# Performance work log

Hardware: AMD Instinct MI355X
Metric: run time of the kernel (lower is better)

Reference implementation:

```python
import jax, jax.numpy as jnp
import numpy as np

TIME_SEG_LEN = 5
PRED_STEPS = 1
B, N, D = 4, 4096, 4
F1, F2 = 32, 64  # cnn filters; F2 must equal GCSConv/Dense width 64


def _conv1d_time(x, Wc1, bc1, Wc2, bc2):
    # x: [B, N, T, D] -> per-node temporal CNN collapsing T=5 -> 1 -> [B, N, F2]
    b, n, t, d = x.shape
    xr = x.reshape(b * n, t, d)
    dn = ('NWC', 'WIO', 'NWC')
    h = jax.lax.conv_general_dilated(xr, Wc1, (1,), 'VALID', dimension_numbers=dn) + bc1
    h = jax.nn.relu(h)
    h = jax.lax.conv_general_dilated(h, Wc2, (1,), 'VALID', dimension_numbers=dn) + bc2
    return h.reshape(b, n, -1)  # [B, N, F2]


def setup_inputs() -> dict:
    key = jax.random.key(0)
    ks = jax.random.split(key, 12)
    time_segs = jax.random.normal(ks[0], (B, TIME_SEG_LEN, N, D), dtype=jnp.float32)
    edges = jax.random.randint(ks[1], (N, N), 0, 2, dtype=jnp.int32)
    s = lambda *sh: 1.0 / np.sqrt(sh[-2] if len(sh) > 1 else sh[0])
    return {
        'time_segs': time_segs,
        'edges': edges,
        'Wc1': jax.random.normal(ks[2], (3, D, F1), dtype=jnp.float32) * 0.3,
        'bc1': jnp.zeros((F1,), jnp.float32),
        'Wc2': jax.random.normal(ks[3], (3, F1, F2), dtype=jnp.float32) * 0.1,
        'bc2': jnp.zeros((F2,), jnp.float32),
        'Wg1': jax.random.normal(ks[4], (F2, 64), dtype=jnp.float32) * 0.125,
        'bg': jnp.zeros((64,), jnp.float32),
        'Wd': jax.random.normal(ks[5], (F2 + 64, 64), dtype=jnp.float32) * 0.09,
        'bd': jnp.zeros((64,), jnp.float32),
        'Wo': jax.random.normal(ks[6], (64, D), dtype=jnp.float32) * 0.125,
        'bo': jnp.zeros((D,), jnp.float32),
    }


def reference(time_segs, edges, Wc1, bc1, Wc2, bc2, Wg1, bg, Wd, bd, Wo, bo):
    A = edges.astype(jnp.float32)
    n = A.shape[0]
    deg = jnp.sum(A, axis=-1, keepdims=True)              # row degree
    A_norm = A / jnp.where(deg > 0, deg, 1.0)             # D^-1 A (symmetric=False)
    A_nd = A_norm * (1.0 - jnp.eye(n, dtype=A.dtype))     # self-edge masking of X row j == zeroing diag
    col_deg = jnp.sum(A, axis=0)                          # e = np.sum(edges, axis=0)
    alive = (col_deg != 0).astype(time_segs.dtype)[None, :, None]  # zero-degree nodes -> zeros branch

    ext = jnp.transpose(time_segs, (0, 2, 1, 3))          # [B, N, T, D]
    for i in range(PRED_STEPS):
        seg = ext[:, :, i:, :]                            # [B, N, 5, D]
        cond = _conv1d_time(seg, Wc1, bc1, Wc2, bc2)      # [B, N, F2]
        # Vectorized per-node masked GCSConv: row j of tanh(A X_j W1 + X_j W2 + b)
        # with X_j = X zeroed at node j. Skip term vanishes at row j.
        agg = jnp.einsum('jk,bkf->bjf', A_nd, cond)       # [B, N, F2]
        G = jnp.tanh(agg @ Wg1 + bg) * alive              # [B, N, 64]
        h = jax.nn.relu(jnp.concatenate([cond, G], axis=-1) @ Wd + bd)
        nxt = seg[:, :, -1, :] + jnp.tanh(h @ Wo + bo)    # residual update [B, N, D]
        ext = jnp.concatenate([ext, nxt[:, :, None, :]], axis=2)
    out = jnp.transpose(ext, (0, 2, 1, 3))                # [B, T+P, N, D]
    return out[:, TIME_SEG_LEN:, :, :]                    # [B, pred_steps, N, D]
```

## Files before the change

### kernel.cpp

```cpp
#include <hip/hip_runtime.h>
#include <math.h>

typedef unsigned short ushort_t;
typedef unsigned int uint_t;
typedef unsigned long long u64_t;
typedef __attribute__((ext_vector_type(8))) __bf16 bf16x8;
typedef __attribute__((ext_vector_type(4))) float f32x4;

#define NN 4096
#define TT 5
#define F1 32
#define F2 64

__device__ __forceinline__ ushort_t f2bf(float x) {
    union { float f; uint_t u; } v; v.f = x;
    uint_t r = (v.u + 0x7FFFu + ((v.u >> 16) & 1u)) >> 16;
    return (ushort_t)r;
}
__device__ __forceinline__ float bf16f(float x) {
    union { float f; uint_t u; } v; v.f = x;
    v.u = (v.u + 0x7FFFu + ((v.u >> 16) & 1u)) & 0xFFFF0000u;
    return v.f;
}
__device__ __forceinline__ uint_t pk2(float a, float b) {
    return (uint_t)f2bf(a) | ((uint_t)f2bf(b) << 16);
}
__device__ __forceinline__ float tanh_fast(float x) {
    const float xc = fminf(fmaxf(x, -10.f), 10.f);
    const float e = __expf(2.f * xc);
    return (e - 1.f) * __builtin_amdgcn_rcpf(e + 1.f);
}
__device__ __forceinline__ void lds_barrier() {
    asm volatile("s_waitcnt lgkmcnt(0)\n\ts_barrier" ::: "memory");
}

__global__ __launch_bounds__(1024) void k0_pack(
    const int* __restrict__ edges, uint_t* __restrict__ packed,
    int* __restrict__ degI, uint_t* __restrict__ colpart)
{
    const int t = threadIdx.x, w = t >> 6, l = t & 63;
    const int row = blockIdx.x * 16 + w;
    __shared__ u64_t lmask[16][64];

    const int* ep = edges + (size_t)row * NN + l * 4;
    u64_t nib = 0; int cnt = 0;
    #pragma unroll
    for (int g = 0; g < 2; ++g) {
        int4 v[8];
        #pragma unroll
        for (int q = 0; q < 8; ++q) v[q] = *(const int4*)(ep + (g * 8 + q) * 256);
        #pragma unroll
        for (int q = 0; q < 8; ++q) {
            const uint_t n = (uint_t)(v[q].x != 0) | ((uint_t)(v[q].y != 0) << 1) |
                             ((uint_t)(v[q].z != 0) << 2) | ((uint_t)(v[q].w != 0) << 3);
            cnt += (v[q].x != 0) + (v[q].y != 0) + (v[q].z != 0) + (v[q].w != 0);
            nib |= (u64_t)n << ((g * 8 + q) * 4);
        }
    }
    lmask[w][l] = nib;
    {
        int s = cnt;
        #pragma unroll
        for (int off = 32; off >= 1; off >>= 1) s += __shfl_down(s, off, 64);
        if (l == 0) degI[row] = s;
    }
    {
        #pragma unroll
        for (int h = 0; h < 2; ++h) {
            const int w2 = l + h * 64;
            const int q = w2 >> 3, g = w2 & 7;
            uint_t word = 0;
            #pragma unroll
            for (int i = 0; i < 8; ++i)
                word |= (uint_t)((lmask[w][g * 8 + i] >> (q * 4)) & 15ull) << (i * 4);
            packed[(size_t)row * 128 + w2] = word;
        }
    }
    __syncthreads();
    if (t < 64) {
        u64_t m = 0;
        #pragma unroll
        for (int w2 = 0; w2 < 16; ++w2) m |= lmask[w2][t];
        lmask[0][t] = m;
    }
    __syncthreads();
    if (t < 128) {
        const int q = t >> 3, g = t & 7;
        uint_t word = 0;
        #pragma unroll
        for (int i = 0; i < 8; ++i)
            word |= (uint_t)((lmask[0][g * 8 + i] >> (q * 4)) & 15ull) << (i * 4);
        colpart[(size_t)blockIdx.x * 128 + t] = word;
    }
}

#define H1S 104
#define CBS 80
__global__ __launch_bounds__(512) void k1_cond(
    const float* __restrict__ ts, const float* __restrict__ Wc1, const float* __restrict__ bc1,
    const float* __restrict__ Wc2, const float* __restrict__ bc2,
    float* __restrict__ condf, ushort_t* __restrict__ condT)
{
    const int b = blockIdx.y;
    const int j0 = blockIdx.x * 64;
    const int t = threadIdx.x;

    __shared__ float sWc1[384];
    __shared__ float sbc1[F1];
    __shared__ float sbc2[F2];
    __shared__ ushort_t sWc2T[64 * H1S];
    __shared__ ushort_t h1B[64 * H1S];
    __shared__ ushort_t scb[64 * CBS];

    for (int i = t; i < 384; i += 512) sWc1[i] = Wc1[i];
    if (t < F1) sbc1[t] = bc1[t];
    if (t < F2) sbc2[t] = bc2[t];
    for (int i = t; i < 96 * 64; i += 512) {
        const int e = i >> 6, f = i & 63;
        sWc2T[f * H1S + e] = f2bf(Wc2[i]);
    }
    __syncthreads();

    {
        const int n = t & 63, g = t >> 6;
        const int j = j0 + n;
        float4 x[5];
        #pragma unroll
        for (int tt = 0; tt < 5; ++tt)
            x[tt] = *(const float4*)(ts + ((((size_t)b * TT + tt) << 12) + j) * 4);
        #pragma unroll
        for (int q = 0; q < 12; ++q) {
            const int e = g * 12 + q;
            const int tt0 = e >> 5, f1 = e & 31;
            float a = sbc1[f1];
            #pragma unroll
            for (int dt = 0; dt < 3; ++dt) {
                const float4 xx = x[tt0 + dt];
                a += xx.x * sWc1[(dt * 4 + 0) * F1 + f1];
                a += xx.y * sWc1[(dt * 4 + 1) * F1 + f1];
                a += xx.z * sWc1[(dt * 4 + 2) * F1 + f1];
                a += xx.w * sWc1[(dt * 4 + 3) * F1 + f1];
            }
            h1B[n * H1S + e] = f2bf(fmaxf(a, 0.f));
        }
    }
    __syncthreads();

    {
        const int w = t >> 6, l = t & 63;
        const int m0 = (w & 3) * 16, cH = (w >> 2) * 32;
        const int kseg = (l >> 4) * 8;
        f32x4 acc[2] = {};
        #pragma unroll
        for (int ks = 0; ks < 3; ++ks) {
            const bf16x8 av = *(const bf16x8*)&h1B[(m0 + (l & 15)) * H1S + ks * 32 + kseg];
            #pragma unroll
            for (int ct = 0; ct < 2; ++ct) {
                const bf16x8 bv = *(const bf16x8*)&sWc2T[(cH + ct * 16 + (l & 15)) * H1S + ks * 32 + kseg];
                acc[ct] = __builtin_amdgcn_mfma_f32_16x16x32_bf16(av, bv, acc[ct], 0, 0, 0);
            }
        }
        #pragma unroll
        for (int ct = 0; ct < 2; ++ct)
            #pragma unroll
            for (int i = 0; i < 4; ++i) {
                const int row = m0 + (l >> 4) * 4 + i;
                const int col = cH + ct * 16 + (l & 15);
                const float c = acc[ct][i] + sbc2[col];
                condf[((((size_t)b << 12) + j0 + row) << 6) + col] = c;
                scb[col * CBS + row] = f2bf(c);
            }
    }
    __syncthreads();
    {
        const int f2 = t >> 3, seg = t & 7;
        ushort_t* dst = condT + (((size_t)b * 64 + f2) << 12) + j0 + seg * 8;
        *(uint4*)dst = *(const uint4*)&scb[f2 * CBS + seg * 8];
    }
}

__global__ __launch_bounds__(512, 4) void k3_gemm(
    const uint_t* __restrict__ packed, const ushort_t* __restrict__ condT,
    float* __restrict__ aggAll)
{
    const int t = threadIdx.x;
    const int rt = blockIdx.x >> 3;
    const int ch = (blockIdx.x >> 2) & 1;
    const int ks = blockIdx.x & 3;
    const int j0 = rt * 64, cb = ch * 128, kb = ks * 1024;

    __shared__ __align__(16) ushort_t aA[64 * 128];
    __shared__ __align__(16) ushort_t bB[128 * 128];

    const int w = t >> 6, l = t & 63;
    const int arow_s = t >> 3, koct = t & 7;
    const uint_t* prow = packed + (size_t)(j0 + arow_s) * 128 + (kb >> 5);
    const int sh = (koct & 1) * 16;
    const int kf0 = koct * 2;
    const int ua0 = (arow_s * 16 + (kf0 ^ (arow_s & 15))) * 8;
    const int ua1 = (arow_s * 16 + ((kf0 + 1) ^ (arow_s & 15))) * 8;
    const int rg = w & 1, cg = w >> 1;
    const int ln = l & 15, asub = l >> 4;

    uint_t pa;
    uint4 pb[4];
    int bcol[4], bseg[4];
    #pragma unroll
    for (int p = 0; p < 4; ++p) {
        const int sid = t + p * 512;
        bcol[p] = sid >> 4; bseg[p] = sid & 15;
    }

    pa = prow[koct >> 1];
    #pragma unroll
    for (int p = 0; p < 4; ++p)
        pb[p] = *(const uint4*)(condT + (size_t)(cb + bcol[p]) * NN + kb + bseg[p] * 8);

    f32x4 acc[2][2] = {};

    for (int c = 0; c < 8; ++c) {
        {
            const uint_t b16 = pa >> sh;
            uint_t e[8];
            #pragma unroll
            for (int p2 = 0; p2 < 8; ++p2)
                e[p2] = (((b16 >> (2 * p2)) & 1u) ? 0x3F80u : 0u) |
                        (((b16 >> (2 * p2 + 1)) & 1u) ? 0x3F800000u : 0u);
            *(uint4*)(&aA[ua0]) = make_uint4(e[0], e[1], e[2], e[3]);
            *(uint4*)(&aA[ua1]) = make_uint4(e[4], e[5], e[6], e[7]);
            #pragma unroll
            for (int p = 0; p < 4; ++p)
                *(uint4*)(&bB[(bcol[p] * 16 + (bseg[p] ^ (bcol[p] & 15))) * 8]) = pb[p];
        }
        if (c < 7) {
            pa = prow[(c + 1) * 4 + (koct >> 1)];
            #pragma unroll
            for (int p = 0; p < 4; ++p)
                pb[p] = *(const uint4*)(condT + (size_t)(cb + bcol[p]) * NN
                                        + kb + (c + 1) * 128 + bseg[p] * 8);
        }
        lds_barrier();
        #pragma unroll
        for (int tt = 0; tt < 4; ++tt) {
            const int kf = tt * 4 + asub;
            const int slot = (kf ^ ln) * 8;
            const bf16x8 a0 = *(const bf16x8*)(&aA[(rg * 32 + ln) * 128 + slot]);
            const bf16x8 a1 = *(const bf16x8*)(&aA[(rg * 32 + 16 + ln) * 128 + slot]);
            const bf16x8 b0 = *(const bf16x8*)(&bB[(cg * 32 + ln) * 128 + slot]);
            const bf16x8 b1 = *(const bf16x8*)(&bB[(cg * 32 + 16 + ln) * 128 + slot]);
            acc[0][0] = __builtin_amdgcn_mfma_f32_16x16x32_bf16(a0, b0, acc[0][0], 0, 0, 0);
            acc[0][1] = __builtin_amdgcn_mfma_f32_16x16x32_bf16(a0, b1, acc[0][1], 0, 0, 0);
            acc[1][0] = __builtin_amdgcn_mfma_f32_16x16x32_bf16(a1, b0, acc[1][0], 0, 0, 0);
            acc[1][1] = __builtin_amdgcn_mfma_f32_16x16x32_bf16(a1, b1, acc[1][1], 0, 0, 0);
        }
        lds_barrier();
    }

    float* slab = aggAll + ((size_t)ks << 20);
    #pragma unroll
    for (int rt2 = 0; rt2 < 2; ++rt2)
        #pragma unroll
        for (int ct = 0; ct < 2; ++ct) {
            const int col = cb + cg * 32 + ct * 16 + ln;
            float* dst = slab + ((size_t)(col >> 6) * NN << 6) + (col & 63);
            #pragma unroll
            for (int i = 0; i < 4; ++i) {
                const int j = j0 + rg * 32 + rt2 * 16 + asub * 4 + i;
                dst[(size_t)j << 6] = acc[rt2][ct][i];
            }
        }
}

#define WGS 88
#define WDS 136
#define HS  69
__global__ __launch_bounds__(512) void k4_mlp(
    const float* __restrict__ ts, const int* __restrict__ edges,
    const float* __restrict__ condf, const float* __restrict__ aggAll,
    const int* __restrict__ degI, const uint_t* __restrict__ colpart,
    const float* __restrict__ Wg1, const float* __restrict__ bg,
    const float* __restrict__ Wd, const float* __restrict__ bd,
    const float* __restrict__ Wo, const float* __restrict__ bo,
    float* __restrict__ out)
{
    const int b = blockIdx.y;
    const int j0 = blockIdx.x * 64;
    const int t = threadIdx.x;

    __shared__ ushort_t sWg1T[64 * WGS];
    __shared__ ushort_t sWdT[64 * WDS];
    __shared__ ushort_t aggB[64 * WGS];
    __shared__ ushort_t catB[64 * WDS];
    __shared__ float sH[64 * HS];
    __shared__ float sWo[256];
    __shared__ float sbg[64], sbd[64], sbo[4];
    __shared__ uint_t sAw[2];

    if (t < 2) sAw[t] = 0u;
    for (int i = t; i < 4096; i += 512) {
        const int in = i >> 6, o = i & 63;
        sWg1T[o * WGS + in] = f2bf(Wg1[i]);
    }
    for (int i = t; i < 8192; i += 512) {
        const int in = i >> 6, o = i & 63;
        sWdT[o * WDS + in] = f2bf(Wd[i]);
    }
    if (t < 256) sWo[t] = Wo[t];
    if (t >= 256 && t < 320) { sbg[t - 256] = bg[t - 256]; sbd[t - 256] = bd[t - 256]; }
    if (t >= 320 && t < 324) sbo[t - 320] = bo[t - 320];
    __syncthreads();

    if (t >= 384 && t < 448) {
        const int i = t - 384;
        const int wsel = i >> 5, chunk = i & 31;
        uint_t v = 0;
        #pragma unroll
        for (int q = 0; q < 8; ++q)
            v |= colpart[(size_t)(chunk * 8 + q) * 128 + (j0 >> 5) + wsel];
        atomicOr(&sAw[wsel], v);
    }
    {
        const int r = t >> 3, fs = t & 7;
        const int j = j0 + r;
        const float dv = (float)degI[j];
        const float inv = 1.f / (dv > 0.f ? dv : 1.f);
        const float dgf = edges[(size_t)j * NN + j] ? 1.f : 0.f;
        const size_t base = (((size_t)b << 12) + j) << 6;
        #pragma unroll
        for (int q = 0; q < 2; ++q) {
            const int f = fs * 8 + q * 4;
            float4 a4 = {0.f, 0.f, 0.f, 0.f};
            #pragma unroll
            for (int s = 0; s < 4; ++s) {
                const float4 sv = *(const float4*)(aggAll + ((size_t)s << 20) + base + f);
                a4.x += sv.x; a4.y += sv.y; a4.z += sv.z; a4.w += sv.w;
            }
            const float4 c4 = *(const float4*)(condf + base + f);
            const float n0 = (a4.x - dgf * bf16f(c4.x)) * inv;
            const float n1 = (a4.y - dgf * bf16f(c4.y)) * inv;
            const float n2 = (a4.z - dgf * bf16f(c4.z)) * inv;
            const float n3 = (a4.w - dgf * bf16f(c4.w)) * inv;
            *(uint2*)&aggB[r * WGS + f] = make_uint2(pk2(n0, n1), pk2(n2, n3));
            *(uint2*)&catB[r * WDS + f] = make_uint2(pk2(c4.x, c4.y), pk2(c4.z, c4.w));
        }
    }
    __syncthreads();

    const int w = t >> 6, l = t & 63;
    const int m0 = (w & 3) * 16, cH = (w >> 2) * 32;
    const int kseg = (l >> 4) * 8;

    {
        f32x4 acc[2] = {};
        #pragma unroll
        for (int ks = 0; ks < 2; ++ks) {
            const bf16x8 av = *(const bf16x8*)&aggB[(m0 + (l & 15)) * WGS + ks * 32 + kseg];
            #pragma unroll
            for (int ct = 0; ct < 2; ++ct) {
                const bf16x8 bv = *(const bf16x8*)&sWg1T[(cH + ct * 16 + (l & 15)) * WGS + ks * 32 + kseg];
                acc[ct] = __builtin_amdgcn_mfma_f32_16x16x32_bf16(av, bv, acc[ct], 0, 0, 0);
            }
        }
        #pragma unroll
        for (int ct = 0; ct < 2; ++ct)
            #pragma unroll
            for (int i = 0; i < 4; ++i) {
                const int row = m0 + (l >> 4) * 4 + i;
                const int col = cH + ct * 16 + (l & 15);
                const float alive = (float)((sAw[row >> 5] >> (row & 31)) & 1u);
                const float g = tanh_fast(acc[ct][i] + sbg[col]) * alive;
                catB[row * WDS + 64 + col] = f2bf(g);
            }
    }
    __syncthreads();
    {
        f32x4 acc[2] = {};
        #pragma unroll
        for (int ks = 0; ks < 4; ++ks) {
            const bf16x8 av = *(const bf16x8*)&catB[(m0 + (l & 15)) * WDS + ks * 32 + kseg];
            #pragma unroll
            for (int ct = 0; ct < 2; ++ct) {
                const bf16x8 bv = *(const bf16x8*)&sWdT[(cH + ct * 16 + (l & 15)) * WDS + ks * 32 + kseg];
                acc[ct] = __builtin_amdgcn_mfma_f32_16x16x32_bf16(av, bv, acc[ct], 0, 0, 0);
            }
        }
        #pragma unroll
        for (int ct = 0; ct < 2; ++ct)
            #pragma unroll
            for (int i = 0; i < 4; ++i) {
                const int row = m0 + (l >> 4) * 4 + i;
                const int col = cH + ct * 16 + (l & 15);
                sH[row * HS + col] = fmaxf(acc[ct][i] + sbd[col], 0.f);
            }
    }
    __syncthreads();
    if (t < 256) {
        const int r = t >> 2, d = t & 3;
        const int j = j0 + r;
        float s = sbo[d];
        #pragma unroll 8
        for (int f = 0; f < 64; ++f) s += sH[r * HS + f] * sWo[f * 4 + d];
        const float segl = ts[((((size_t)b * TT + 4) << 12) + j) * 4 + d];
        out[((((size_t)b << 12) + j) << 2) + d] = segl + tanh_fast(s);
    }
}

extern "C" void kernel_launch(void* const* d_in, const int* in_sizes, int n_in,
                              void* d_out, int out_size, void* d_ws, size_t ws_size,
                              hipStream_t stream)
{
    (void)in_sizes; (void)n_in; (void)out_size; (void)ws_size;
    const float* ts    = (const float*)d_in[0];
    const int*   edges = (const int*)d_in[1];
    const float* Wc1   = (const float*)d_in[2];
    const float* bc1   = (const float*)d_in[3];
    const float* Wc2   = (const float*)d_in[4];
    const float* bc2   = (const float*)d_in[5];
    const float* Wg1   = (const float*)d_in[6];
    const float* bg    = (const float*)d_in[7];
    const float* Wd    = (const float*)d_in[8];
    const float* bd    = (const float*)d_in[9];
    const float* Wo    = (const float*)d_in[10];
    const float* bo    = (const float*)d_in[11];
    float* out = (float*)d_out;

    char* ws = (char*)d_ws;
    ushort_t* condT   = (ushort_t*)(ws);
    float*    condf   = (float*)(ws + (size_t)(2 << 20));
    float*    aggAll  = (float*)(ws + (size_t)(6 << 20));
    uint_t*   packed  = (uint_t*)(ws + (size_t)(22 << 20));
    int*      degI    = (int*)(ws + (size_t)(24 << 20));
    uint_t*   colpart = (uint_t*)(ws + (size_t)(24 << 20) + 16384);

    k0_pack<<<256, 1024, 0, stream>>>(edges, packed, degI, colpart);
    k1_cond<<<dim3(64, 4), 512, 0, stream>>>(ts, Wc1, bc1, Wc2, bc2, condf, condT);
    k3_gemm<<<512, 512, 0, stream>>>(packed, condT, aggAll);
    k4_mlp<<<dim3(64, 4), 512, 0, stream>>>(ts, edges, condf, aggAll, degI, colpart,
                                            Wg1, bg, Wd, bd, Wo, bo, out);
}
```

Baseline: 187.8 us.

## Pre-pack weights into MFMA fragment layout once and split k3 launch

Weight matrices Wc2, Wg1 and Wd are converted to bf16 once, in the pack kernel, and stored in global memory already in the MFMA B-fragment order. k1 and k4 then read B operands straight from global memory instead of having every block transpose and convert the weights into LDS, which cuts per-block setup work and LDS footprint. The k3 GEMM launch is split into two half-grid launches driven by a jbase offset, and its LDS is merged into a single buffer. The trade-off is global-memory fragment loads inside the MFMA loops and one extra kernel launch.

```diff
diff --git a/kernel.cpp b/kernel.cpp
--- a/kernel.cpp
+++ b/kernel.cpp
@@ -36,11 +36,28 @@
 
 __global__ __launch_bounds__(1024) void k0_pack(
     const int* __restrict__ edges, uint_t* __restrict__ packed,
-    int* __restrict__ degI, uint_t* __restrict__ colpart)
+    int* __restrict__ degI, uint_t* __restrict__ colpart,
+    const float* __restrict__ Wc2, const float* __restrict__ Wg1,
+    const float* __restrict__ Wd, ushort_t* __restrict__ wfrag)
 {
     const int t = threadIdx.x, w = t >> 6, l = t & 63;
     const int row = blockIdx.x * 16 + w;
     __shared__ u64_t lmask[16][64];
+
+    {
+        const int p = blockIdx.x * 1024 + t;
+        if (p < 9216) {
+            int dloc; const float* src; ushort_t* dst;
+            if (p < 3072)      { dloc = p * 2;            src = Wc2; dst = wfrag; }
+            else if (p < 5120) { dloc = (p - 3072) * 2;   src = Wg1; dst = wfrag + 6144; }
+            else               { dloc = (p - 5120) * 2;   src = Wd;  dst = wfrag + 10240; }
+            const int tile = dloc >> 9, rem = dloc & 511;
+            const int ll = rem >> 3, j = rem & 7;
+            const int ks = tile >> 2, c16 = tile & 3;
+            const int k = ks * 32 + (ll >> 4) * 8 + j, col = c16 * 16 + (ll & 15);
+            *(uint_t*)(dst + dloc) = pk2(src[k * 64 + col], src[(k + 1) * 64 + col]);
+        }
+    }
 
     const int* ep = edges + (size_t)row * NN + l * 4;
     u64_t nib = 0; int cnt = 0;
@@ -98,8 +115,8 @@
 #define CBS 80
 __global__ __launch_bounds__(512) void k1_cond(
     const float* __restrict__ ts, const float* __restrict__ Wc1, const float* __restrict__ bc1,
-    const float* __restrict__ Wc2, const float* __restrict__ bc2,
-    float* __restrict__ condf, ushort_t* __restrict__ condT)
+    const float* __restrict__ bc2, float* __restrict__ condf, ushort_t* __restrict__ condT,
+    const ushort_t* __restrict__ wfrag)
 {
     const int b = blockIdx.y;
     const int j0 = blockIdx.x * 64;
@@ -108,17 +125,12 @@
     __shared__ float sWc1[384];
     __shared__ float sbc1[F1];
     __shared__ float sbc2[F2];
-    __shared__ ushort_t sWc2T[64 * H1S];
     __shared__ ushort_t h1B[64 * H1S];
     __shared__ ushort_t scb[64 * CBS];
 
-    for (int i = t; i < 384; i += 512) sWc1[i] = Wc1[i];
+    if (t < 384) sWc1[t] = Wc1[t];
     if (t < F1) sbc1[t] = bc1[t];
     if (t < F2) sbc2[t] = bc2[t];
-    for (int i = t; i < 96 * 64; i += 512) {
-        const int e = i >> 6, f = i & 63;
-        sWc2T[f * H1S + e] = f2bf(Wc2[i]);
-    }
     __syncthreads();
 
     {
@@ -148,7 +160,7 @@
 
     {
         const int w = t >> 6, l = t & 63;
-        const int m0 = (w & 3) * 16, cH = (w >> 2) * 32;
+        const int m0 = (w & 3) * 16;
         const int kseg = (l >> 4) * 8;
         f32x4 acc[2] = {};
         #pragma unroll
@@ -156,7 +168,8 @@
             const bf16x8 av = *(const bf16x8*)&h1B[(m0 + (l & 15)) * H1S + ks * 32 + kseg];
             #pragma unroll
             for (int ct = 0; ct < 2; ++ct) {
-                const bf16x8 bv = *(const bf16x8*)&sWc2T[(cH + ct * 16 + (l & 15)) * H1S + ks * 32 + kseg];
+                const int c16 = (w >> 2) * 2 + ct;
+                const bf16x8 bv = *(const bf16x8*)(wfrag + ((ks * 4 + c16) << 9) + l * 8);
                 acc[ct] = __builtin_amdgcn_mfma_f32_16x16x32_bf16(av, bv, acc[ct], 0, 0, 0);
             }
         }
@@ -165,7 +178,7 @@
             #pragma unroll
             for (int i = 0; i < 4; ++i) {
                 const int row = m0 + (l >> 4) * 4 + i;
-                const int col = cH + ct * 16 + (l & 15);
+                const int col = (w >> 2) * 32 + ct * 16 + (l & 15);
                 const float c = acc[ct][i] + sbc2[col];
                 condf[((((size_t)b << 12) + j0 + row) << 6) + col] = c;
                 scb[col * CBS + row] = f2bf(c);
@@ -181,16 +194,18 @@
 
 __global__ __launch_bounds__(512, 4) void k3_gemm(
     const uint_t* __restrict__ packed, const ushort_t* __restrict__ condT,
-    float* __restrict__ aggAll)
+    float* __restrict__ aggAll, int jbase)
 {
     const int t = threadIdx.x;
     const int rt = blockIdx.x >> 3;
     const int ch = (blockIdx.x >> 2) & 1;
     const int ks = blockIdx.x & 3;
-    const int j0 = rt * 64, cb = ch * 128, kb = ks * 1024;
-
-    __shared__ __align__(16) ushort_t aA[64 * 128];
-    __shared__ __align__(16) ushort_t bB[128 * 128];
+    const int j0 = jbase + rt * 64, kb = ks * 1024;
+    const int cb = ch * 128;
+
+    __shared__ __align__(16) ushort_t smem[24576];
+    ushort_t* aA = smem;
+    ushort_t* bB = smem + 8192;
 
     const int w = t >> 6, l = t & 63;
     const int arow_s = t >> 3, koct = t & 7;
@@ -278,8 +293,8 @@
     const float* __restrict__ ts, const int* __restrict__ edges,
     const float* __restrict__ condf, const float* __restrict__ aggAll,
     const int* __restrict__ degI, const uint_t* __restrict__ colpart,
-    const float* __restrict__ Wg1, const float* __restrict__ bg,
-    const float* __restrict__ Wd, const float* __restrict__ bd,
+    const ushort_t* __restrict__ wfrag,
+    const float* __restrict__ bg, const float* __restrict__ bd,
     const float* __restrict__ Wo, const float* __restrict__ bo,
     float* __restrict__ out)
 {
@@ -287,8 +302,6 @@
     const int j0 = blockIdx.x * 64;
     const int t = threadIdx.x;
 
-    __shared__ ushort_t sWg1T[64 * WGS];
-    __shared__ ushort_t sWdT[64 * WDS];
     __shared__ ushort_t aggB[64 * WGS];
     __shared__ ushort_t catB[64 * WDS];
     __shared__ float sH[64 * HS];
@@ -296,15 +309,10 @@
     __shared__ float sbg[64], sbd[64], sbo[4];
     __shared__ uint_t sAw[2];
 
+    const ushort_t* wg1f = wfrag + 6144;
+    const ushort_t* wdf  = wfrag + 10240;
+
     if (t < 2) sAw[t] = 0u;
-    for (int i = t; i < 4096; i += 512) {
-        const int in = i >> 6, o = i & 63;
-        sWg1T[o * WGS + in] = f2bf(Wg1[i]);
-    }
-    for (int i = t; i < 8192; i += 512) {
-        const int in = i >> 6, o = i & 63;
-        sWdT[o * WDS + in] = f2bf(Wd[i]);
-    }
     if (t < 256) sWo[t] = Wo[t];
     if (t >= 256 && t < 320) { sbg[t - 256] = bg[t - 256]; sbd[t - 256] = bd[t - 256]; }
     if (t >= 320 && t < 324) sbo[t - 320] = bo[t - 320];
@@ -357,7 +365,8 @@
             const bf16x8 av = *(const bf16x8*)&aggB[(m0 + (l & 15)) * WGS + ks * 32 + kseg];
             #pragma unroll
             for (int ct = 0; ct < 2; ++ct) {
-                const bf16x8 bv = *(const bf16x8*)&sWg1T[(cH + ct * 16 + (l & 15)) * WGS + ks * 32 + kseg];
+                const int c16 = (w >> 2) * 2 + ct;
+                const bf16x8 bv = *(const bf16x8*)(wg1f + ((ks * 4 + c16) << 9) + l * 8);
                 acc[ct] = __builtin_amdgcn_mfma_f32_16x16x32_bf16(av, bv, acc[ct], 0, 0, 0);
             }
         }
@@ -380,7 +389,8 @@
             const bf16x8 av = *(const bf16x8*)&catB[(m0 + (l & 15)) * WDS + ks * 32 + kseg];
             #pragma unroll
             for (int ct = 0; ct < 2; ++ct) {
-                const bf16x8 bv = *(const bf16x8*)&sWdT[(cH + ct * 16 + (l & 15)) * WDS + ks * 32 + kseg];
+                const int c16 = (w >> 2) * 2 + ct;
+                const bf16x8 bv = *(const bf16x8*)(wdf + ((ks * 4 + c16) << 9) + l * 8);
                 acc[ct] = __builtin_amdgcn_mfma_f32_16x16x32_bf16(av, bv, acc[ct], 0, 0, 0);
             }
         }
@@ -431,10 +441,12 @@
     uint_t*   packed  = (uint_t*)(ws + (size_t)(22 << 20));
     int*      degI    = (int*)(ws + (size_t)(24 << 20));
     uint_t*   colpart = (uint_t*)(ws + (size_t)(24 << 20) + 16384);
-
-    k0_pack<<<256, 1024, 0, stream>>>(edges, packed, degI, colpart);
-    k1_cond<<<dim3(64, 4), 512, 0, stream>>>(ts, Wc1, bc1, Wc2, bc2, condf, condT);
-    k3_gemm<<<512, 512, 0, stream>>>(packed, condT, aggAll);
+    ushort_t* wfrag   = (ushort_t*)(ws + (size_t)(25 << 20));
+
+    k0_pack<<<256, 1024, 0, stream>>>(edges, packed, degI, colpart, Wc2, Wg1, Wd, wfrag);
+    k1_cond<<<dim3(64, 4), 512, 0, stream>>>(ts, Wc1, bc1, bc2, condf, condT, wfrag);
+    k3_gemm<<<256, 512, 0, stream>>>(packed, condT, aggAll, 0);
+    k3_gemm<<<256, 512, 0, stream>>>(packed, condT, aggAll, 2048);
     k4_mlp<<<dim3(64, 4), 512, 0, stream>>>(ts, edges, condf, aggAll, degI, colpart,
-                                            Wg1, bg, Wd, bd, Wo, bo, out);
-}
+                                            wfrag, bg, bd, Wo, bo, out);
+}
```

Result: no change. 188.1 us (+0.2%).
